# Kernel optimization log

Measured on AMD Instinct MI355X. Metric: run time of the kernel, lower is better.

The kernel has to match this reference:

```python
import jax, jax.numpy as jnp
import numpy as np

HUGE = 1e9  # stand-in for ops.HUGE_INT


def setup_inputs() -> dict:
    key = jax.random.key(0)
    ks = jax.random.split(key, 8)
    B, Q, K = 8, 128, 256
    Dq = Dk = Dv = H = 512
    query = jax.random.normal(ks[0], (B, Q, Dq), dtype=jnp.float32)
    k_ = jax.random.normal(ks[1], (B, K, Dk), dtype=jnp.float32)
    value = jax.random.normal(ks[2], (B, K, Dv), dtype=jnp.float32)
    mask = jax.random.randint(ks[3], (B, K), 0, 2, dtype=jnp.int32)
    # FFN params: linear1 (Dq+Dk -> H, bias), linear2 (H -> 1, no bias)
    W1 = jax.random.normal(ks[4], (Dq + Dk, H), dtype=jnp.float32) * 0.05
    b1 = jax.random.normal(ks[5], (H,), dtype=jnp.float32) * 0.05
    w2 = jax.random.normal(ks[6], (H, 1), dtype=jnp.float32) * 0.05
    return {"query": query, "key": k_, "value": value, "mask": mask,
            "W1": W1, "b1": b1, "w2": w2}


def reference(query, key, value, mask, W1, b1, w2):
    # Additive (FFN) attention. Original tiles query/key into [B, Q*K, Dq+Dk]
    # and applies linear1; concat@W1 is separable, so we project q and k
    # separately and broadcast-add (same math, no tiled concat tensor).
    Dq = query.shape[-1]
    Wq, Wk = W1[:Dq], W1[Dq:]
    q_proj = jnp.einsum('bqd,dh->bqh', query, Wq)   # [B,Q,H]
    k_proj = jnp.einsum('bkd,dh->bkh', key, Wk)     # [B,K,H]
    hidden = jnp.tanh(q_proj[:, :, None, :] + k_proj[:, None, :, :] + b1)  # [B,Q,K,H]
    scores = jnp.einsum('bqkh,h->bqk', hidden, w2[:, 0])  # [B,Q,K]
    # padding mask fill BEFORE scaling, matching the original op order
    scores = jnp.where(mask[:, None, :] != 0, -HUGE, scores)
    scores = scores / jnp.sqrt(jnp.float32(key.shape[-1]))
    attn_weights = jax.nn.softmax(scores, axis=-1)
    attn_vec = jnp.einsum('bqk,bkv->bqv', attn_weights, value)  # dropout=0 at eval
    return attn_vec, attn_weights
```

## Files before the change

### kernel.cpp

```cpp
#include <hip/hip_runtime.h>
#include <hip/hip_bf16.h>

#define B_ 8
#define Q_ 128
#define K_ 256
#define D_ 512
#define TWOLOG2E 2.8853900817779268f
#define SCALE 0.044194173824159216f
#define L2E 1.4426950408889634f
#define MASKVAL (-44194173.824159216f)

typedef __attribute__((ext_vector_type(8))) short frag8;
typedef __attribute__((ext_vector_type(4))) float f32x4;

__device__ __forceinline__ float fexp2(float x) {
  float r;
  asm("v_exp_f32 %0, %1" : "=v"(r) : "v"(x));
  return r;
}
__device__ __forceinline__ float frcp(float x) {
  float r;
  asm("v_rcp_f32 %0, %1" : "=v"(r) : "v"(x));
  return r;
}
__device__ __forceinline__ unsigned f2bf_u(float x) {
  unsigned u = __float_as_uint(x);
  return (u + 0x7FFFu + ((u >> 16) & 1u)) >> 16;
}
__device__ __forceinline__ unsigned short f2bf(float x) {
  return (unsigned short)f2bf_u(x);
}
__device__ __forceinline__ unsigned packbf(float lo, float hi) {
  return f2bf_u(lo) | (f2bf_u(hi) << 16);
}

__global__ __launch_bounds__(256) void gemm_kernel(
    const float* __restrict__ query, const float* __restrict__ key,
    const float* __restrict__ W1, const float* __restrict__ b1,
    float* __restrict__ qp, float* __restrict__ kpbT) {
  __shared__ short As[32 * 64];
  __shared__ short Bs[64 * 72];
  const int t = threadIdx.x;
  const int m0 = blockIdx.y * 32;
  const int n0 = blockIdx.x * 64;
  const bool is_k = (m0 >= B_ * Q_);
  const float* X = is_k ? key : query;
  const int xrow0 = is_k ? (m0 - B_ * Q_) : m0;
  const float* Wb = W1 + (is_k ? (size_t)D_ * D_ : 0);

  const int am = t >> 3;
  const int ac = t & 7;
  const float* gA = X + (size_t)(xrow0 + am) * D_ + ac * 8;
  short* aw = As + am * 64 + ((ac ^ (am & 7)) * 8);

  const int prow = t >> 4;
  const int n4 = (t & 15) * 4;
  const float* gB = Wb + n0 + n4;

  const int l = t & 63;
  const int w = t >> 6;
  const int lr = l & 15;
  const int kg = l >> 4;
  const int key8 = lr & 7;
  int aoff[2][2], boff[2];
#pragma unroll
  for (int kk = 0; kk < 2; ++kk) {
    const int cposA = ((kg + kk * 4) ^ key8) * 8;
#pragma unroll
    for (int mt = 0; mt < 2; ++mt) aoff[mt][kk] = (mt * 16 + lr) * 64 + cposA;
    boff[kk] = (w * 16 + lr) * 72 + (kg + kk * 4) * 8;
  }

  f32x4 acc[2];
  acc[0] = (f32x4){0.f, 0.f, 0.f, 0.f};
  acc[1] = (f32x4){0.f, 0.f, 0.f, 0.f};

  for (int k0 = 0; k0 < D_; k0 += 64) {
    float4 a0 = *(const float4*)(gA + k0);
    float4 a1 = *(const float4*)(gA + k0 + 4);
    float4 w00 = *(const float4*)(gB + (size_t)(k0 + 2 * prow) * D_);
    float4 w01 = *(const float4*)(gB + (size_t)(k0 + 2 * prow + 1) * D_);
    float4 w10 = *(const float4*)(gB + (size_t)(k0 + 2 * prow + 32) * D_);
    float4 w11 = *(const float4*)(gB + (size_t)(k0 + 2 * prow + 33) * D_);
    __syncthreads();
    {
      union { frag8 f; unsigned short u[8]; } av;
      av.u[0] = f2bf(a0.x); av.u[1] = f2bf(a0.y); av.u[2] = f2bf(a0.z); av.u[3] = f2bf(a0.w);
      av.u[4] = f2bf(a1.x); av.u[5] = f2bf(a1.y); av.u[6] = f2bf(a1.z); av.u[7] = f2bf(a1.w);
      *(frag8*)aw = av.f;
    }
    {
      float lo0[4] = {w00.x, w00.y, w00.z, w00.w};
      float hi0[4] = {w01.x, w01.y, w01.z, w01.w};
      float lo1[4] = {w10.x, w10.y, w10.z, w10.w};
      float hi1[4] = {w11.x, w11.y, w11.z, w11.w};
#pragma unroll
      for (int j = 0; j < 4; ++j) {
        *(unsigned*)(Bs + (n4 + j) * 72 + 2 * prow) = packbf(lo0[j], hi0[j]);
        *(unsigned*)(Bs + (n4 + j) * 72 + 2 * (prow + 16)) = packbf(lo1[j], hi1[j]);
      }
    }
    __syncthreads();
#pragma unroll
    for (int kk = 0; kk < 2; ++kk) {
      frag8 bf = *(const frag8*)(Bs + boff[kk]);
#pragma unroll
      for (int mt = 0; mt < 2; ++mt) {
        frag8 af = *(const frag8*)(As + aoff[mt][kk]);
        acc[mt] = __builtin_amdgcn_mfma_f32_16x16x32_bf16(af, bf, acc[mt], 0, 0, 0);
      }
    }
  }

  const int col = n0 + w * 16 + lr;
  if (is_k) {
    const float bc = b1[col];
#pragma unroll
    for (int mt = 0; mt < 2; ++mt) {
      const int krow = m0 - B_ * Q_ + mt * 16 + kg * 4;
      const int bb = krow >> 8;
      const int kk0 = krow & 255;
      float4 v;
      v.x = fexp2((acc[mt][0] + bc) * TWOLOG2E);
      v.y = fexp2((acc[mt][1] + bc) * TWOLOG2E);
      v.z = fexp2((acc[mt][2] + bc) * TWOLOG2E);
      v.w = fexp2((acc[mt][3] + bc) * TWOLOG2E);
      *(float4*)&kpbT[((size_t)bb * D_ + col) * K_ + kk0] = v;
    }
  } else {
#pragma unroll
    for (int mt = 0; mt < 2; ++mt) {
#pragma unroll
      for (int i = 0; i < 4; ++i) {
        const int row = m0 + mt * 16 + kg * 4 + i;
        qp[(size_t)row * D_ + col] = fexp2(acc[mt][i] * TWOLOG2E);
      }
    }
  }
}

__global__ __launch_bounds__(1024) void attn_kernel(
    const float* __restrict__ qp, const float* __restrict__ kpbT,
    const float* __restrict__ value, const int* __restrict__ mask,
    const float* __restrict__ w2,
    float* __restrict__ out_vec, float* __restrict__ out_w) {
  __shared__ float smem_p[16 * 256];
  __shared__ float pw[4 * 256];
  const int b = blockIdx.y;
  const int q0 = blockIdx.x * 4;
  const int t = threadIdx.x;
  const int lane = t & 63;
  const int w = __builtin_amdgcn_readfirstlane(t >> 6);
  const int kc = w & 3;
  const int hq = w >> 2;

  {
    const float* pk = kpbT + ((size_t)b * D_ + hq * 128) * K_ + kc * 64 + lane;
    const float* q_0 = qp + (size_t)(b * Q_ + q0 + 0) * D_ + hq * 128;
    const float* q_1 = qp + (size_t)(b * Q_ + q0 + 1) * D_ + hq * 128;
    const float* q_2 = qp + (size_t)(b * Q_ + q0 + 2) * D_ + hq * 128;
    const float* q_3 = qp + (size_t)(b * Q_ + q0 + 3) * D_ + hq * 128;
    const float* w2h = w2 + hq * 128;

    float a0 = 0.f, a1 = 0.f, a2 = 0.f, a3 = 0.f;
    for (int h = 0; h < 128; h += 8) {
      float kv[8];
#pragma unroll
      for (int j = 0; j < 8; ++j) kv[j] = pk[(size_t)(h + j) * K_];
      float4 e0a = *(const float4*)(q_0 + h), e0b = *(const float4*)(q_0 + h + 4);
      float4 e1a = *(const float4*)(q_1 + h), e1b = *(const float4*)(q_1 + h + 4);
      float4 e2a = *(const float4*)(q_2 + h), e2b = *(const float4*)(q_2 + h + 4);
      float4 e3a = *(const float4*)(q_3 + h), e3b = *(const float4*)(q_3 + h + 4);
      float4 wa = *(const float4*)(w2h + h), wb = *(const float4*)(w2h + h + 4);
      float E0[8] = {e0a.x, e0a.y, e0a.z, e0a.w, e0b.x, e0b.y, e0b.z, e0b.w};
      float E1[8] = {e1a.x, e1a.y, e1a.z, e1a.w, e1b.x, e1b.y, e1b.z, e1b.w};
      float E2[8] = {e2a.x, e2a.y, e2a.z, e2a.w, e2b.x, e2b.y, e2b.z, e2b.w};
      float E3[8] = {e3a.x, e3a.y, e3a.z, e3a.w, e3b.x, e3b.y, e3b.z, e3b.w};
      float WV[8] = {wa.x, wa.y, wa.z, wa.w, wb.x, wb.y, wb.z, wb.w};
#pragma unroll
      for (int j = 0; j < 8; ++j) {
        const float r0 = frcp(fmaf(E0[j], kv[j], 1.f));
        const float r1 = frcp(fmaf(E1[j], kv[j], 1.f));
        const float r2 = frcp(fmaf(E2[j], kv[j], 1.f));
        const float r3 = frcp(fmaf(E3[j], kv[j], 1.f));
        a0 = fmaf(WV[j], r0, a0);
        a1 = fmaf(WV[j], r1, a1);
        a2 = fmaf(WV[j], r2, a2);
        a3 = fmaf(WV[j], r3, a3);
      }
    }
    smem_p[w * 256 + 0 * 64 + lane] = a0;
    smem_p[w * 256 + 1 * 64 + lane] = a1;
    smem_p[w * 256 + 2 * 64 + lane] = a2;
    smem_p[w * 256 + 3 * 64 + lane] = a3;
  }
  __syncthreads();

  if (w < 4) {
    float sw = 0.f;
#pragma unroll
    for (int m = 0; m < 8; ++m) sw += w2[lane + 64 * m];
#pragma unroll
    for (int off = 32; off; off >>= 1) sw += __shfl_xor(sw, off);

    float s[4];
#pragma unroll
    for (int r = 0; r < 4; ++r) {
      float p = smem_p[(0 * 4 + r) * 256 + w * 64 + lane] +
                smem_p[(1 * 4 + r) * 256 + w * 64 + lane] +
                smem_p[(2 * 4 + r) * 256 + w * 64 + lane] +
                smem_p[(3 * 4 + r) * 256 + w * 64 + lane];
      const int mk = mask[b * K_ + r * 64 + lane];
      s[r] = mk ? MASKVAL : fmaf(-2.f, p, sw) * SCALE;
    }
    float mx = fmaxf(fmaxf(s[0], s[1]), fmaxf(s[2], s[3]));
#pragma unroll
    for (int off = 32; off; off >>= 1) mx = fmaxf(mx, __shfl_xor(mx, off));
    float e[4], sum = 0.f;
#pragma unroll
    for (int r = 0; r < 4; ++r) {
      e[r] = fexp2((s[r] - mx) * L2E);
      sum += e[r];
    }
#pragma unroll
    for (int off = 32; off; off >>= 1) sum += __shfl_xor(sum, off);
    const float inv = frcp(sum);
    float* ow = out_w + (size_t)(b * Q_ + q0 + w) * K_;
#pragma unroll
    for (int r = 0; r < 4; ++r) {
      const float p = e[r] * inv;
      pw[w * 256 + r * 64 + lane] = p;
      ow[r * 64 + lane] = p;
    }
  }
  __syncthreads();

  const int col = t & 511;
  const int qq = t >> 9;
  float o0 = 0.f, o1 = 0.f;
  const float* vb = value + (size_t)b * K_ * D_;
  for (int k = 0; k < K_; k += 4) {
    const float4 p0 = *(const float4*)&pw[(qq * 2 + 0) * 256 + k];
    const float4 p1 = *(const float4*)&pw[(qq * 2 + 1) * 256 + k];
    const float v0 = vb[(size_t)(k + 0) * D_ + col];
    const float v1 = vb[(size_t)(k + 1) * D_ + col];
    const float v2 = vb[(size_t)(k + 2) * D_ + col];
    const float v3 = vb[(size_t)(k + 3) * D_ + col];
    o0 = fmaf(p0.x, v0, fmaf(p0.y, v1, fmaf(p0.z, v2, fmaf(p0.w, v3, o0))));
    o1 = fmaf(p1.x, v0, fmaf(p1.y, v1, fmaf(p1.z, v2, fmaf(p1.w, v3, o1))));
  }
  out_vec[(size_t)(b * Q_ + q0 + qq * 2 + 0) * D_ + col] = o0;
  out_vec[(size_t)(b * Q_ + q0 + qq * 2 + 1) * D_ + col] = o1;
}

extern "C" void kernel_launch(void* const* d_in, const int* in_sizes, int n_in,
                              void* d_out, int out_size, void* d_ws, size_t ws_size,
                              hipStream_t stream) {
  const float* query = (const float*)d_in[0];
  const float* key   = (const float*)d_in[1];
  const float* value = (const float*)d_in[2];
  const int*   mask  = (const int*)d_in[3];
  const float* W1    = (const float*)d_in[4];
  const float* b1    = (const float*)d_in[5];
  const float* w2    = (const float*)d_in[6];

  float* out_vec = (float*)d_out;
  float* out_w   = out_vec + (size_t)B_ * Q_ * D_;

  float* qp   = (float*)d_ws;
  float* kpbT = qp + (size_t)B_ * Q_ * D_;

  gemm_kernel<<<dim3(8, 96), 256, 0, stream>>>(query, key, W1, b1, qp, kpbT);
  attn_kernel<<<dim3(Q_ / 4, B_), 1024, 0, stream>>>(qp, kpbT, value, mask, w2,
                                                     out_vec, out_w);
}
```

Before: 113.3 us.

## Compact unmasked keys and compute scores only for them, halving queries per block

Wavefront 0 builds a compacted list of unmasked key indices with ballot/popcount, and the tanh-FFN score loop now covers only those keys. The wave split between key chunks and hidden slices adapts to the unmasked count. Masked keys get the mask value written straight into shared memory. Each block now handles 2 queries instead of 4, giving twice as many blocks. This targets the rcp-heavy score loop, since about half the keys are masked, at the cost of a gather via the index list and less reuse of key loads across queries.

```diff
diff --git a/kernel.cpp b/kernel.cpp
--- a/kernel.cpp
+++ b/kernel.cpp
@@ -139,97 +139,117 @@
   }
 }
 
-__global__ __launch_bounds__(1024) void attn_kernel(
+__global__ __launch_bounds__(1024, 8) void attn_kernel(
     const float* __restrict__ qp, const float* __restrict__ kpbT,
     const float* __restrict__ value, const int* __restrict__ mask,
     const float* __restrict__ w2,
     float* __restrict__ out_vec, float* __restrict__ out_w) {
-  __shared__ float smem_p[16 * 256];
-  __shared__ float pw[4 * 256];
+  __shared__ int idxl[K_];
+  __shared__ int sM;
+  __shared__ float smem_p[16 * 2 * 64];
+  __shared__ float pw[2 * K_];
   const int b = blockIdx.y;
-  const int q0 = blockIdx.x * 4;
+  const int q0 = blockIdx.x * 2;
   const int t = threadIdx.x;
   const int lane = t & 63;
   const int w = __builtin_amdgcn_readfirstlane(t >> 6);
-  const int kc = w & 3;
-  const int hq = w >> 2;
+
+  if (w == 0) {
+    int base = 0;
+#pragma unroll
+    for (int c = 0; c < 4; ++c) {
+      const int k = c * 64 + lane;
+      const int mk = mask[b * K_ + k];
+      const unsigned long long bal = __ballot(mk == 0);
+      const int pos = __popcll(bal & ((1ull << lane) - 1ull));
+      if (mk == 0) idxl[base + pos] = k;
+      base += (int)__popcll(bal);
+    }
+    if (lane == 0) sM = base;
+  }
+  __syncthreads();
+
+  const int M = sM;
+  const int s = (M > 128) ? 2 : (M > 64) ? 1 : 0;
+  const int kchunks = 1 << s;
 
   {
-    const float* pk = kpbT + ((size_t)b * D_ + hq * 128) * K_ + kc * 64 + lane;
-    const float* q_0 = qp + (size_t)(b * Q_ + q0 + 0) * D_ + hq * 128;
-    const float* q_1 = qp + (size_t)(b * Q_ + q0 + 1) * D_ + hq * 128;
-    const float* q_2 = qp + (size_t)(b * Q_ + q0 + 2) * D_ + hq * 128;
-    const float* q_3 = qp + (size_t)(b * Q_ + q0 + 3) * D_ + hq * 128;
-    const float* w2h = w2 + hq * 128;
-
-    float a0 = 0.f, a1 = 0.f, a2 = 0.f, a3 = 0.f;
-    for (int h = 0; h < 128; h += 8) {
+    const int kc = w & (kchunks - 1);
+    const int hsel = w >> s;
+    const int hlen = 32 << s;
+    const int h0 = hsel * hlen;
+
+    const int slot = kc * 64 + lane;
+    const int sl = (slot < M) ? slot : (M > 0 ? M - 1 : 0);
+    const int kk = idxl[sl] & 255;
+
+    const float* pk = kpbT + ((size_t)b * D_ + h0) * K_ + kk;
+    const float* q_0 = qp + (size_t)(b * Q_ + q0 + 0) * D_ + h0;
+    const float* q_1 = qp + (size_t)(b * Q_ + q0 + 1) * D_ + h0;
+    const float* w2h = w2 + h0;
+
+    float a0 = 0.f, a1 = 0.f;
+    for (int h = 0; h < hlen; h += 8) {
       float kv[8];
 #pragma unroll
       for (int j = 0; j < 8; ++j) kv[j] = pk[(size_t)(h + j) * K_];
       float4 e0a = *(const float4*)(q_0 + h), e0b = *(const float4*)(q_0 + h + 4);
       float4 e1a = *(const float4*)(q_1 + h), e1b = *(const float4*)(q_1 + h + 4);
-      float4 e2a = *(const float4*)(q_2 + h), e2b = *(const float4*)(q_2 + h + 4);
-      float4 e3a = *(const float4*)(q_3 + h), e3b = *(const float4*)(q_3 + h + 4);
       float4 wa = *(const float4*)(w2h + h), wb = *(const float4*)(w2h + h + 4);
       float E0[8] = {e0a.x, e0a.y, e0a.z, e0a.w, e0b.x, e0b.y, e0b.z, e0b.w};
       float E1[8] = {e1a.x, e1a.y, e1a.z, e1a.w, e1b.x, e1b.y, e1b.z, e1b.w};
-      float E2[8] = {e2a.x, e2a.y, e2a.z, e2a.w, e2b.x, e2b.y, e2b.z, e2b.w};
-      float E3[8] = {e3a.x, e3a.y, e3a.z, e3a.w, e3b.x, e3b.y, e3b.z, e3b.w};
       float WV[8] = {wa.x, wa.y, wa.z, wa.w, wb.x, wb.y, wb.z, wb.w};
 #pragma unroll
       for (int j = 0; j < 8; ++j) {
         const float r0 = frcp(fmaf(E0[j], kv[j], 1.f));
         const float r1 = frcp(fmaf(E1[j], kv[j], 1.f));
-        const float r2 = frcp(fmaf(E2[j], kv[j], 1.f));
-        const float r3 = frcp(fmaf(E3[j], kv[j], 1.f));
         a0 = fmaf(WV[j], r0, a0);
         a1 = fmaf(WV[j], r1, a1);
-        a2 = fmaf(WV[j], r2, a2);
-        a3 = fmaf(WV[j], r3, a3);
-      }
-    }
-    smem_p[w * 256 + 0 * 64 + lane] = a0;
-    smem_p[w * 256 + 1 * 64 + lane] = a1;
-    smem_p[w * 256 + 2 * 64 + lane] = a2;
-    smem_p[w * 256 + 3 * 64 + lane] = a3;
+      }
+    }
+    smem_p[w * 128 + 0 * 64 + lane] = a0;
+    smem_p[w * 128 + 1 * 64 + lane] = a1;
   }
   __syncthreads();
 
-  if (w < 4) {
+  if (w < 2) {
+    const int q = w;
     float sw = 0.f;
 #pragma unroll
     for (int m = 0; m < 8; ++m) sw += w2[lane + 64 * m];
 #pragma unroll
     for (int off = 32; off; off >>= 1) sw += __shfl_xor(sw, off);
 
-    float s[4];
-#pragma unroll
-    for (int r = 0; r < 4; ++r) {
-      float p = smem_p[(0 * 4 + r) * 256 + w * 64 + lane] +
-                smem_p[(1 * 4 + r) * 256 + w * 64 + lane] +
-                smem_p[(2 * 4 + r) * 256 + w * 64 + lane] +
-                smem_p[(3 * 4 + r) * 256 + w * 64 + lane];
-      const int mk = mask[b * K_ + r * 64 + lane];
-      s[r] = mk ? MASKVAL : fmaf(-2.f, p, sw) * SCALE;
-    }
-    float mx = fmaxf(fmaxf(s[0], s[1]), fmaxf(s[2], s[3]));
+#pragma unroll
+    for (int r = 0; r < 4; ++r) pw[q * K_ + r * 64 + lane] = MASKVAL;
+    for (int r = 0; r < kchunks; ++r) {
+      float p = 0.f;
+      for (int v = 0; v < (16 >> s); ++v)
+        p += smem_p[(((v << s) | r) * 2 + q) * 64 + lane];
+      const int slot = r * 64 + lane;
+      if (slot < M) pw[q * K_ + idxl[slot]] = fmaf(-2.f, p, sw) * SCALE;
+    }
+
+    float sv[4];
+#pragma unroll
+    for (int r = 0; r < 4; ++r) sv[r] = pw[q * K_ + r * 64 + lane];
+    float mx = fmaxf(fmaxf(sv[0], sv[1]), fmaxf(sv[2], sv[3]));
 #pragma unroll
     for (int off = 32; off; off >>= 1) mx = fmaxf(mx, __shfl_xor(mx, off));
     float e[4], sum = 0.f;
 #pragma unroll
     for (int r = 0; r < 4; ++r) {
-      e[r] = fexp2((s[r] - mx) * L2E);
+      e[r] = fexp2((sv[r] - mx) * L2E);
       sum += e[r];
     }
 #pragma unroll
     for (int off = 32; off; off >>= 1) sum += __shfl_xor(sum, off);
     const float inv = frcp(sum);
-    float* ow = out_w + (size_t)(b * Q_ + q0 + w) * K_;
+    float* ow = out_w + (size_t)(b * Q_ + q0 + q) * K_;
 #pragma unroll
     for (int r = 0; r < 4; ++r) {
       const float p = e[r] * inv;
-      pw[w * 256 + r * 64 + lane] = p;
+      pw[q * K_ + r * 64 + lane] = p;
       ow[r * 64 + lane] = p;
     }
   }
@@ -237,20 +257,17 @@
 
   const int col = t & 511;
   const int qq = t >> 9;
-  float o0 = 0.f, o1 = 0.f;
+  float o = 0.f;
   const float* vb = value + (size_t)b * K_ * D_;
   for (int k = 0; k < K_; k += 4) {
-    const float4 p0 = *(const float4*)&pw[(qq * 2 + 0) * 256 + k];
-    const float4 p1 = *(const float4*)&pw[(qq * 2 + 1) * 256 + k];
+    const float4 p = *(const float4*)&pw[qq * K_ + k];
     const float v0 = vb[(size_t)(k + 0) * D_ + col];
     const float v1 = vb[(size_t)(k + 1) * D_ + col];
     const float v2 = vb[(size_t)(k + 2) * D_ + col];
     const float v3 = vb[(size_t)(k + 3) * D_ + col];
-    o0 = fmaf(p0.x, v0, fmaf(p0.y, v1, fmaf(p0.z, v2, fmaf(p0.w, v3, o0))));
-    o1 = fmaf(p1.x, v0, fmaf(p1.y, v1, fmaf(p1.z, v2, fmaf(p1.w, v3, o1))));
-  }
-  out_vec[(size_t)(b * Q_ + q0 + qq * 2 + 0) * D_ + col] = o0;
-  out_vec[(size_t)(b * Q_ + q0 + qq * 2 + 1) * D_ + col] = o1;
+    o = fmaf(p.x, v0, fmaf(p.y, v1, fmaf(p.z, v2, fmaf(p.w, v3, o))));
+  }
+  out_vec[(size_t)(b * Q_ + q0 + qq) * D_ + col] = o;
 }
 
 extern "C" void kernel_launch(void* const* d_in, const int* in_sizes, int n_in,
@@ -271,6 +288,6 @@
   float* kpbT = qp + (size_t)B_ * Q_ * D_;
 
   gemm_kernel<<<dim3(8, 96), 256, 0, stream>>>(query, key, W1, b1, qp, kpbT);
-  attn_kernel<<<dim3(Q_ / 4, B_), 1024, 0, stream>>>(qp, kpbT, value, mask, w2,
+  attn_kernel<<<dim3(Q_ / 2, B_), 1024, 0, stream>>>(qp, kpbT, value, mask, w2,
                                                      out_vec, out_w);
 }
```

After: 124.4 us. 1.1x slower.

## Give each lane two key columns in score loop to double q-projection reuse

Applied to the files above, without the earlier changes.

Changes the score-phase work split from 4 key chunks × 4 hidden quarters to 2 key chunks × 8 hidden slices of 64. Each lane now handles two adjacent keys through float2 loads, so every loaded q-projection and w2 value feeds twice as many rcp/FMA operations. The cost is a larger shared partial buffer and an 8-way reduction in the softmax step. More live accumulators may also raise register pressure in the 1024-thread block.

```diff
diff --git a/kernel.cpp b/kernel.cpp
--- a/kernel.cpp
+++ b/kernel.cpp
@@ -144,29 +144,30 @@
     const float* __restrict__ value, const int* __restrict__ mask,
     const float* __restrict__ w2,
     float* __restrict__ out_vec, float* __restrict__ out_w) {
-  __shared__ float smem_p[16 * 256];
+  __shared__ float smem_p[16 * 512];
   __shared__ float pw[4 * 256];
   const int b = blockIdx.y;
   const int q0 = blockIdx.x * 4;
   const int t = threadIdx.x;
   const int lane = t & 63;
   const int w = __builtin_amdgcn_readfirstlane(t >> 6);
-  const int kc = w & 3;
-  const int hq = w >> 2;
+  const int kc = w & 1;
+  const int hq = w >> 1;
+  const int h0 = hq * 64;
 
   {
-    const float* pk = kpbT + ((size_t)b * D_ + hq * 128) * K_ + kc * 64 + lane;
-    const float* q_0 = qp + (size_t)(b * Q_ + q0 + 0) * D_ + hq * 128;
-    const float* q_1 = qp + (size_t)(b * Q_ + q0 + 1) * D_ + hq * 128;
-    const float* q_2 = qp + (size_t)(b * Q_ + q0 + 2) * D_ + hq * 128;
-    const float* q_3 = qp + (size_t)(b * Q_ + q0 + 3) * D_ + hq * 128;
-    const float* w2h = w2 + hq * 128;
-
-    float a0 = 0.f, a1 = 0.f, a2 = 0.f, a3 = 0.f;
-    for (int h = 0; h < 128; h += 8) {
-      float kv[8];
-#pragma unroll
-      for (int j = 0; j < 8; ++j) kv[j] = pk[(size_t)(h + j) * K_];
+    const float* pk = kpbT + ((size_t)b * D_ + h0) * K_ + kc * 128 + 2 * lane;
+    const float* q_0 = qp + (size_t)(b * Q_ + q0 + 0) * D_ + h0;
+    const float* q_1 = qp + (size_t)(b * Q_ + q0 + 1) * D_ + h0;
+    const float* q_2 = qp + (size_t)(b * Q_ + q0 + 2) * D_ + h0;
+    const float* q_3 = qp + (size_t)(b * Q_ + q0 + 3) * D_ + h0;
+    const float* w2h = w2 + h0;
+
+    float2 a0 = {0.f, 0.f}, a1 = {0.f, 0.f}, a2 = {0.f, 0.f}, a3 = {0.f, 0.f};
+    for (int h = 0; h < 64; h += 8) {
+      float2 kv[8];
+#pragma unroll
+      for (int j = 0; j < 8; ++j) kv[j] = *(const float2*)&pk[(size_t)(h + j) * K_];
       float4 e0a = *(const float4*)(q_0 + h), e0b = *(const float4*)(q_0 + h + 4);
       float4 e1a = *(const float4*)(q_1 + h), e1b = *(const float4*)(q_1 + h + 4);
       float4 e2a = *(const float4*)(q_2 + h), e2b = *(const float4*)(q_2 + h + 4);
@@ -179,24 +180,25 @@
       float WV[8] = {wa.x, wa.y, wa.z, wa.w, wb.x, wb.y, wb.z, wb.w};
 #pragma unroll
       for (int j = 0; j < 8; ++j) {
-        const float r0 = frcp(fmaf(E0[j], kv[j], 1.f));
-        const float r1 = frcp(fmaf(E1[j], kv[j], 1.f));
-        const float r2 = frcp(fmaf(E2[j], kv[j], 1.f));
-        const float r3 = frcp(fmaf(E3[j], kv[j], 1.f));
-        a0 = fmaf(WV[j], r0, a0);
-        a1 = fmaf(WV[j], r1, a1);
-        a2 = fmaf(WV[j], r2, a2);
-        a3 = fmaf(WV[j], r3, a3);
-      }
-    }
-    smem_p[w * 256 + 0 * 64 + lane] = a0;
-    smem_p[w * 256 + 1 * 64 + lane] = a1;
-    smem_p[w * 256 + 2 * 64 + lane] = a2;
-    smem_p[w * 256 + 3 * 64 + lane] = a3;
+        a0.x = fmaf(WV[j], frcp(fmaf(E0[j], kv[j].x, 1.f)), a0.x);
+        a0.y = fmaf(WV[j], frcp(fmaf(E0[j], kv[j].y, 1.f)), a0.y);
+        a1.x = fmaf(WV[j], frcp(fmaf(E1[j], kv[j].x, 1.f)), a1.x);
+        a1.y = fmaf(WV[j], frcp(fmaf(E1[j], kv[j].y, 1.f)), a1.y);
+        a2.x = fmaf(WV[j], frcp(fmaf(E2[j], kv[j].x, 1.f)), a2.x);
+        a2.y = fmaf(WV[j], frcp(fmaf(E2[j], kv[j].y, 1.f)), a2.y);
+        a3.x = fmaf(WV[j], frcp(fmaf(E3[j], kv[j].x, 1.f)), a3.x);
+        a3.y = fmaf(WV[j], frcp(fmaf(E3[j], kv[j].y, 1.f)), a3.y);
+      }
+    }
+    *(float2*)&smem_p[w * 512 + 0 * 128 + 2 * lane] = a0;
+    *(float2*)&smem_p[w * 512 + 1 * 128 + 2 * lane] = a1;
+    *(float2*)&smem_p[w * 512 + 2 * 128 + 2 * lane] = a2;
+    *(float2*)&smem_p[w * 512 + 3 * 128 + 2 * lane] = a3;
   }
   __syncthreads();
 
   if (w < 4) {
+    const int q = w;
     float sw = 0.f;
 #pragma unroll
     for (int m = 0; m < 8; ++m) sw += w2[lane + 64 * m];
@@ -206,10 +208,12 @@
     float s[4];
 #pragma unroll
     for (int r = 0; r < 4; ++r) {
-      float p = smem_p[(0 * 4 + r) * 256 + w * 64 + lane] +
-                smem_p[(1 * 4 + r) * 256 + w * 64 + lane] +
-                smem_p[(2 * 4 + r) * 256 + w * 64 + lane] +
-                smem_p[(3 * 4 + r) * 256 + w * 64 + lane];
+      const int kcc = r >> 1;
+      const int off = (r & 1) * 64 + lane;
+      float p = 0.f;
+#pragma unroll
+      for (int hh = 0; hh < 8; ++hh)
+        p += smem_p[(hh * 2 + kcc) * 512 + q * 128 + off];
       const int mk = mask[b * K_ + r * 64 + lane];
       s[r] = mk ? MASKVAL : fmaf(-2.f, p, sw) * SCALE;
     }
@@ -225,11 +229,11 @@
 #pragma unroll
     for (int off = 32; off; off >>= 1) sum += __shfl_xor(sum, off);
     const float inv = frcp(sum);
-    float* ow = out_w + (size_t)(b * Q_ + q0 + w) * K_;
+    float* ow = out_w + (size_t)(b * Q_ + q0 + q) * K_;
 #pragma unroll
     for (int r = 0; r < 4; ++r) {
       const float p = e[r] * inv;
-      pw[w * 256 + r * 64 + lane] = p;
+      pw[q * 256 + r * 64 + lane] = p;
       ow[r * 64 + lane] = p;
     }
   }
```

After: 111.6 us. Within noise of the previous version (-1.5%).
